# Kernel tuning notes

Measured on AMD Instinct MI355X. Metric: run time of the kernel, lower is better.

## Reference

```python
import jax, jax.numpy as jnp
import numpy as np
from jax import lax

DN = ('NCHW', 'OIHW', 'NCHW')


def setup_inputs() -> dict:
    key = jax.random.key(0)
    k1, k2, k3, k4, k5, k6 = jax.random.split(key, 6)
    B, Ch, H, W = 16, 256, 32, 32   # two feature maps of 256 ch -> c = 512
    C = 2 * Ch
    return {
        'x1': jax.random.normal(k1, (B, Ch, H, W), dtype=jnp.float32),
        'x2': jax.random.normal(k2, (B, Ch, H, W), dtype=jnp.float32),
        'g_w': jax.random.normal(k3, (C, C, 3, 3), dtype=jnp.float32) * 0.02,
        'w_w': jax.random.normal(k4, (256, C, 1, 1), dtype=jnp.float32) * 0.05,
        'weight1': jax.random.normal(k5, (C, 16), dtype=jnp.float32) * 0.1,
        'weight2': jax.random.normal(k6, (C, 16), dtype=jnp.float32) * 0.1,
    }


def reference(x1, x2, g_w, w_w, weight1, weight2):
    x = jnp.concatenate([x1, x2], axis=1)            # [b, c, h, w]
    b, c, h, w = x.shape
    g_x = lax.conv_general_dilated(x, g_w, (1, 1), 'SAME', dimension_numbers=DN)
    value = g_x.reshape(b, c, h * w)                 # [b, c, n]
    q = x.reshape(b, c, h * w)                       # query == key source
    sim = jnp.einsum('bcn,bdn->bcd', q, q) * (float(c) ** -0.5)  # [b, c, c]
    random_map = weight1 @ weight2.T                 # [c, c]
    attn = jax.nn.softmax(sim + random_map[None], axis=-1)
    ctx = jnp.einsum('bcd,bdn->bcn', attn, value).reshape(b, c, h, w)
    out = lax.conv_general_dilated(ctx, w_w, (1, 1), 'VALID', dimension_numbers=DN)
    return out
```

## Files before the change

kernel.cpp:

```cpp
#include <hip/hip_runtime.h>
#include <math.h>

typedef float f32x4 __attribute__((ext_vector_type(4)));
typedef short s16x8 __attribute__((ext_vector_type(8)));
typedef unsigned int u32;
typedef unsigned short u16;
typedef u16 u16x4 __attribute__((ext_vector_type(4)));

static constexpr size_t OFF_XT    = 0;
static constexpr size_t OFF_XQ    = 4734976;
static constexpr size_t OFF_ATTNT = 8929280;
static constexpr size_t OFF_SIMT  = 11026432;
static constexpr size_t OFF_WA    = 13123584;
static constexpr size_t OFF_RM    = 14303232;
static constexpr size_t OFF_WWB   = 14565376;

__device__ __forceinline__ u16 f2bf(float f) {
    u32 u = __float_as_uint(f);
    u32 r = (u + 0x7FFFu + ((u >> 16) & 1u)) >> 16;
    return (u16)r;
}
__device__ __forceinline__ float bf2f(u16 v) {
    return __uint_as_float(((u32)v) << 16);
}

__device__ __forceinline__ void gload_lds16(const void* g, void* l) {
    __builtin_amdgcn_global_load_lds(
        (const u32 __attribute__((address_space(1)))*)(uintptr_t)g,
        (u32 __attribute__((address_space(3)))*)(uintptr_t)l, 16, 0, 0);
}

__global__ __launch_bounds__(256) void prep_kernel(const float* __restrict__ x1,
                                                   const float* __restrict__ x2,
                                                   const float* __restrict__ gw,
                                                   const float* __restrict__ ww,
                                                   const float* __restrict__ w1,
                                                   const float* __restrict__ w2,
                                                   float* __restrict__ rm,
                                                   u16* __restrict__ wA,
                                                   u16* __restrict__ wwb,
                                                   u16* __restrict__ xT,
                                                   u16* __restrict__ xq) {
    __shared__ __attribute__((aligned(16))) u32 shm[4608];
    const int t = threadIdx.x;
    const int bid = blockIdx.x;

    if (bid < 512) {
        const int co = bid;
        const float* g = gw + (size_t)co * 4608;
        float* lf = (float*)shm;
#pragma unroll
        for (int i = 0; i < 18; ++i) lf[t + i * 256] = g[t + i * 256];
        __syncthreads();
        u16* dst = wA + (size_t)co * 4608;
#pragma unroll
        for (int i = 0; i < 18; ++i) {
            int k = t + i * 256;
            int r = k >> 9, ci = k & 511;
            dst[k] = f2bf(lf[ci * 9 + r]);
        }
    } else if (bid < 2560) {
        int xid = bid - 512;
        int nt = xid & 15;
        int cit = (xid >> 4) & 7;
        int b = xid >> 7;
        int n0 = nt * 64, ci0 = cit * 64;
        const float* src = (ci0 < 256) ? (x1 + ((size_t)(b * 256 + ci0)) * 1024)
                                       : (x2 + ((size_t)(b * 256 + ci0 - 256)) * 1024);
        u16* xqb = xq + ((size_t)(b * 512 + ci0)) * 1024;
        u16* lt = (u16*)shm;
#pragma unroll
        for (int p4 = 0; p4 < 4; ++p4) {
            int ch = (t >> 4) + p4 * 16;
            int px = (t & 15) * 4;
            float4 v = *(const float4*)&src[(size_t)ch * 1024 + n0 + px];
            u16x4 pk = {f2bf(v.x), f2bf(v.y), f2bf(v.z), f2bf(v.w)};
            *(u16x4*)&xqb[(size_t)ch * 1024 + n0 + px] = pk;
            lt[(px + 0) * 65 + ch] = pk[0];
            lt[(px + 1) * 65 + ch] = pk[1];
            lt[(px + 2) * 65 + ch] = pk[2];
            lt[(px + 3) * 65 + ch] = pk[3];
        }
        __syncthreads();
        {
            int px_l = t >> 2, c16 = (t & 3) * 16;
            int n = n0 + px_l;
            int y = n >> 5, x = n & 31;
            int p = (y + 1) * 34 + (x + 1);
            u16* dst = xT + ((size_t)b * 1156 + p) * 512 + ci0 + c16;
            *(s16x8*)&dst[0] = *(const s16x8*)&lt[px_l * 65 + c16];
            *(s16x8*)&dst[8] = *(const s16x8*)&lt[px_l * 65 + c16 + 8];
        }
    } else if (bid < 2576) {
        int b = bid - 2560;
        u16* base = xT + (size_t)b * 1156 * 512;
        s16x8 z = {0, 0, 0, 0, 0, 0, 0, 0};
        for (int idx = t; idx < 132 * 64; idx += 256) {
            int row = idx >> 6, seg = idx & 63;
            int p;
            if (row < 34) p = row;
            else if (row < 68) p = 1122 + (row - 34);
            else if (row < 100) p = (row - 67) * 34;
            else p = (row - 99) * 34 + 33;
            *(s16x8*)&base[(size_t)p * 512 + seg * 8] = z;
        }
    } else if (bid < 3600) {
        int idx = (bid - 2576) * 256 + t;
        int c = idx >> 9, d = idx & 511;
        float s = 0.f;
#pragma unroll
        for (int k = 0; k < 16; ++k) s = fmaf(w1[c * 16 + k], w2[d * 16 + k], s);
        rm[idx] = s;
    } else {
        int idx = (bid - 3600) * 256 + t;
        float4 v = ((const float4*)ww)[idx];
        u16x4 pk = {f2bf(v.x), f2bf(v.y), f2bf(v.z), f2bf(v.w)};
        *(u16x4*)&wwb[(size_t)idx * 4] = pk;
    }
}

__global__ __launch_bounds__(256) void sim_gemm(const u16* __restrict__ xq,
                                                const float* __restrict__ rm,
                                                u16* __restrict__ simT) {
    __shared__ __attribute__((aligned(16))) u16 smem[128 * 128];
    u16* As = smem;
    u16* Bs = smem + 128 * 64;
    const int b = blockIdx.z, m0 = blockIdx.y * 128, n0 = blockIdx.x * 128;
    const int t = threadIdx.x, w = t >> 6, l = t & 63;
    const u16* xb = xq + (size_t)b * 512 * 1024;

    const u16 *agp[4], *bgp[4];
    u16 *ald[4], *bld[4];
#pragma unroll
    for (int i = 0; i < 4; ++i) {
        int rr = w * 8 + i * 32 + (l >> 3);
        int gi = (l & 7) ^ (rr & 7);
        agp[i] = xb + (size_t)(m0 + rr) * 1024 + gi * 8;
        bgp[i] = xb + (size_t)(n0 + rr) * 1024 + gi * 8;
        ald[i] = &As[(w * 8 + i * 32) * 64];
        bld[i] = &Bs[(w * 8 + i * 32) * 64];
    }

    f32x4 acc[4][4] = {};
    const int wm = (w >> 1) * 64, wn = (w & 1) * 64;

    for (int kt = 0; kt < 16; ++kt) {
        int ko = kt << 6;
        if (kt) __syncthreads();
#pragma unroll
        for (int i = 0; i < 4; ++i) gload_lds16(agp[i] + ko, ald[i]);
#pragma unroll
        for (int i = 0; i < 4; ++i) gload_lds16(bgp[i] + ko, bld[i]);
        __syncthreads();
#pragma unroll
        for (int kk = 0; kk < 2; ++kk) {
            int gbase = kk * 4 + (l >> 4);
            s16x8 af[4], bf[4];
#pragma unroll
            for (int i = 0; i < 4; ++i) {
                int row = wm + i * 16 + (l & 15);
                af[i] = *(const s16x8*)&As[row * 64 + ((gbase ^ (row & 7)) << 3)];
            }
#pragma unroll
            for (int j = 0; j < 4; ++j) {
                int row = wn + j * 16 + (l & 15);
                bf[j] = *(const s16x8*)&Bs[row * 64 + ((gbase ^ (row & 7)) << 3)];
            }
#pragma unroll
            for (int i = 0; i < 4; ++i)
#pragma unroll
                for (int j = 0; j < 4; ++j)
                    acc[i][j] = __builtin_amdgcn_mfma_f32_16x16x32_bf16(af[i], bf[j], acc[i][j], 0, 0, 0);
        }
    }

    __syncthreads();
    const int col = l & 15, r4 = (l >> 4) * 4;
    const float scale = 0.04419417382415922f;
#pragma unroll
    for (int i = 0; i < 4; ++i)
#pragma unroll
        for (int j = 0; j < 4; ++j) {
            int n_l = wn + j * 16 + col;
            int m_b = wm + i * 16 + r4;
            u16x4 pk;
#pragma unroll
            for (int reg = 0; reg < 4; ++reg) {
                float v = acc[i][j][reg] * scale
                        + rm[(size_t)(m0 + m_b + reg) * 512 + (n0 + n_l)];
                pk[reg] = f2bf(v);
            }
            *(u16x4*)&smem[n_l * 128 + (m_b ^ ((n_l & 15) << 3))] = pk;
        }
    __syncthreads();
    u16* sTb = simT + (size_t)b * 512 * 512;
    {
        int n_l = t >> 1;
#pragma unroll
        for (int rep = 0; rep < 8; ++rep) {
            int c0 = (((t & 1) + rep * 2) << 3);
            s16x8 v = *(const s16x8*)&smem[n_l * 128 + (c0 ^ ((n_l & 15) << 3))];
            *(s16x8*)&sTb[(size_t)(n0 + n_l) * 512 + m0 + c0] = v;
        }
    }
}

__global__ __launch_bounds__(256) void softmax_t(const u16* __restrict__ simT,
                                                 u16* __restrict__ attnT) {
    __shared__ float scr[256];
    const int t = threadIdx.x;
    const int b = blockIdx.x >> 4, c0 = (blockIdx.x & 15) * 32;
    const int cl = t & 31, g = t >> 5;
    const u16* sp = simT + (size_t)b * 512 * 512 + c0 + cl;
    u16* ap = attnT + (size_t)b * 512 * 512 + c0 + cl;

    float s = 0.f;
#pragma unroll 8
    for (int dd = 0; dd < 64; ++dd) {
        int d = g * 64 + dd;
        s += __expf(bf2f(sp[(size_t)d * 512]));
    }
    scr[t] = s;
    __syncthreads();
    float tot = 0.f;
#pragma unroll
    for (int k = 0; k < 8; ++k) tot += scr[k * 32 + cl];
    float inv = 1.f / tot;
#pragma unroll 8
    for (int dd = 0; dd < 64; ++dd) {
        int d = g * 64 + dd;
        float e = __expf(bf2f(sp[(size_t)d * 512])) * inv;
        ap[(size_t)d * 512] = f2bf(e);
    }
}

__global__ __launch_bounds__(256) void conv_gemm(const u16* __restrict__ wA,
                                                 const u16* __restrict__ xT,
                                                 u16* __restrict__ vT) {
    __shared__ __attribute__((aligned(16))) u16 smem[128 * 128];
    u16* As = smem;
    u16* Bs = smem + 128 * 64;
    const int b = blockIdx.z, m0 = blockIdx.y * 128, n0 = blockIdx.x * 128;
    const int t = threadIdx.x, w = t >> 6, l = t & 63;
    const u16* xTb = xT + (size_t)b * 1156 * 512;

    int gi[4], pb[4];
    const u16* agp[4];
    u16 *ald[4], *bld[4];
#pragma unroll
    for (int i = 0; i < 4; ++i) {
        int rr = w * 8 + i * 32 + (l >> 3);
        gi[i] = (l & 7) ^ (rr & 7);
        agp[i] = wA + (size_t)(m0 + rr) * 4608 + gi[i] * 8;
        int n = n0 + rr;
        pb[i] = (n >> 5) * 34 + (n & 31);
        ald[i] = &As[(w * 8 + i * 32) * 64];
        bld[i] = &Bs[(w * 8 + i * 32) * 64];
    }

    f32x4 acc[4][4] = {};
    const int wm = (w >> 1) * 64, wn = (w & 1) * 64;

    for (int kt = 0; kt < 72; ++kt) {
        int r = kt >> 3, ci0k = (kt & 7) << 6;
        int rdiv3 = (r * 11) >> 5;
        int poff = rdiv3 * 34 + (r - rdiv3 * 3);
        int aofs = r * 512 + ci0k;
        if (kt) __syncthreads();
#pragma unroll
        for (int i = 0; i < 4; ++i) gload_lds16(agp[i] + aofs, ald[i]);
#pragma unroll
        for (int i = 0; i < 4; ++i)
            gload_lds16(xTb + (size_t)(pb[i] + poff) * 512 + ci0k + gi[i] * 8, bld[i]);
        __syncthreads();

#pragma unroll
        for (int kk = 0; kk < 2; ++kk) {
            int gbase = kk * 4 + (l >> 4);
            s16x8 af[4], bf[4];
#pragma unroll
            for (int i = 0; i < 4; ++i) {
                int row = wm + i * 16 + (l & 15);
                af[i] = *(const s16x8*)&As[row * 64 + ((gbase ^ (row & 7)) << 3)];
            }
#pragma unroll
            for (int j = 0; j < 4; ++j) {
                int row = wn + j * 16 + (l & 15);
                bf[j] = *(const s16x8*)&Bs[row * 64 + ((gbase ^ (row & 7)) << 3)];
            }
#pragma unroll
            for (int i = 0; i < 4; ++i)
#pragma unroll
                for (int j = 0; j < 4; ++j)
                    acc[i][j] = __builtin_amdgcn_mfma_f32_16x16x32_bf16(af[i], bf[j], acc[i][j], 0, 0, 0);
        }
    }

    __syncthreads();
    const int col = l & 15, r4 = (l >> 4) * 4;
#pragma unroll
    for (int i = 0; i < 4; ++i)
#pragma unroll
        for (int j = 0; j < 4; ++j) {
            int n_l = wn + j * 16 + col;
            int co_b = wm + i * 16 + r4;
            u16x4 pk = {f2bf(acc[i][j][0]), f2bf(acc[i][j][1]),
                        f2bf(acc[i][j][2]), f2bf(acc[i][j][3])};
            *(u16x4*)&smem[n_l * 128 + (co_b ^ ((n_l & 15) << 3))] = pk;
        }
    __syncthreads();
    u16* vTb = vT + (size_t)b * 1024 * 512;
    {
        int n_l = t >> 1;
#pragma unroll
        for (int rep = 0; rep < 8; ++rep) {
            int c0 = (((t & 1) + rep * 2) << 3);
            s16x8 v = *(const s16x8*)&smem[n_l * 128 + (c0 ^ ((n_l & 15) << 3))];
            *(s16x8*)&vTb[(size_t)(n0 + n_l) * 512 + m0 + c0] = v;
        }
    }
}

template <int MODE>
__global__ __launch_bounds__(256) void gemm_nt(const u16* __restrict__ A, size_t sA,
                                               const u16* __restrict__ B, size_t sB,
                                               void* __restrict__ Cv, size_t sC,
                                               int K, int ldc) {
    __shared__ __attribute__((aligned(16))) u16 As[128 * 64];
    __shared__ __attribute__((aligned(16))) u16 Bs[128 * 64];
    const int b = blockIdx.z, m0 = blockIdx.y * 128, n0 = blockIdx.x * 128;
    const int t = threadIdx.x, w = t >> 6, l = t & 63;
    const u16* Ab = A + (size_t)b * sA;
    const u16* Bb = B + (size_t)b * sB;

    const u16 *agp[4], *bgp[4];
    u16 *ald[4], *bld[4];
#pragma unroll
    for (int i = 0; i < 4; ++i) {
        int rr = w * 8 + i * 32 + (l >> 3);
        int gi = (l & 7) ^ (rr & 7);
        agp[i] = Ab + (size_t)(m0 + rr) * K + gi * 8;
        bgp[i] = Bb + (size_t)(n0 + rr) * K + gi * 8;
        ald[i] = &As[(w * 8 + i * 32) * 64];
        bld[i] = &Bs[(w * 8 + i * 32) * 64];
    }

    f32x4 acc[4][4] = {};
    const int wm = (w >> 1) * 64, wn = (w & 1) * 64;
    const int nkt = K >> 6;
    for (int kt = 0; kt < nkt; ++kt) {
        int ko = kt << 6;
        if (kt) __syncthreads();
#pragma unroll
        for (int i = 0; i < 4; ++i) gload_lds16(agp[i] + ko, ald[i]);
#pragma unroll
        for (int i = 0; i < 4; ++i) gload_lds16(bgp[i] + ko, bld[i]);
        __syncthreads();
#pragma unroll
        for (int kk = 0; kk < 2; ++kk) {
            int gbase = kk * 4 + (l >> 4);
            s16x8 af[4], bf[4];
#pragma unroll
            for (int i = 0; i < 4; ++i) {
                int row = wm + i * 16 + (l & 15);
                af[i] = *(const s16x8*)&As[row * 64 + ((gbase ^ (row & 7)) << 3)];
            }
#pragma unroll
            for (int j = 0; j < 4; ++j) {
                int row = wn + j * 16 + (l & 15);
                bf[j] = *(const s16x8*)&Bs[row * 64 + ((gbase ^ (row & 7)) << 3)];
            }
#pragma unroll
            for (int i = 0; i < 4; ++i)
#pragma unroll
                for (int j = 0; j < 4; ++j)
                    acc[i][j] = __builtin_amdgcn_mfma_f32_16x16x32_bf16(af[i], bf[j], acc[i][j], 0, 0, 0);
        }
    }

    const int col = l & 15, r4 = (l >> 4) * 4;
#pragma unroll
    for (int i = 0; i < 4; ++i)
#pragma unroll
        for (int j = 0; j < 4; ++j)
#pragma unroll
            for (int reg = 0; reg < 4; ++reg) {
                int m = m0 + wm + i * 16 + r4 + reg;
                int n = n0 + wn + j * 16 + col;
                if (MODE == 1) {
                    u16* C = (u16*)Cv + (size_t)b * sC;
                    C[(size_t)m * ldc + n] = f2bf(acc[i][j][reg]);
                } else {
                    float* C = (float*)Cv + (size_t)b * sC;
                    C[(size_t)m * ldc + n] = acc[i][j][reg];
                }
            }
}

extern "C" void kernel_launch(void* const* d_in, const int* in_sizes, int n_in,
                              void* d_out, int out_size, void* d_ws, size_t ws_size,
                              hipStream_t stream) {
    (void)in_sizes; (void)n_in; (void)out_size; (void)ws_size;
    const float* x1 = (const float*)d_in[0];
    const float* x2 = (const float*)d_in[1];
    const float* gw = (const float*)d_in[2];
    const float* ww = (const float*)d_in[3];
    const float* w1 = (const float*)d_in[4];
    const float* w2 = (const float*)d_in[5];
    float* out = (float*)d_out;
    float* ws = (float*)d_ws;

    u16* xT    = (u16*)(ws + OFF_XT);
    u16* xq    = (u16*)(ws + OFF_XQ);
    u16* vT    = (u16*)(ws + OFF_XQ);
    u16* attnT = (u16*)(ws + OFF_ATTNT);
    u16* simT  = (u16*)(ws + OFF_SIMT);
    u16* wattn = (u16*)(ws + OFF_SIMT);
    u16* wA    = (u16*)(ws + OFF_WA);
    float* rm  = ws + OFF_RM;
    u16* wwb   = (u16*)(ws + OFF_WWB);

    prep_kernel<<<3728, 256, 0, stream>>>(x1, x2, gw, ww, w1, w2, rm, wA, wwb, xT, xq);
    sim_gemm<<<dim3(4, 4, 16), 256, 0, stream>>>(xq, rm, simT);
    softmax_t<<<256, 256, 0, stream>>>(simT, attnT);
    gemm_nt<1><<<dim3(4, 2, 16), 256, 0, stream>>>(
        wwb, 0, attnT, (size_t)512 * 512, wattn, (size_t)256 * 512, 512, 512);
    conv_gemm<<<dim3(8, 4, 16), 256, 0, stream>>>(wA, xT, vT);
    gemm_nt<2><<<dim3(8, 2, 16), 256, 0, stream>>>(
        wattn, (size_t)256 * 512, vT, (size_t)1024 * 512, out, (size_t)256 * 1024, 512, 1024);
}
```

Before: 234.0 us.

## Split sim GEMM over K into two partials and fuse reduction into softmax

The sim GEMM is split-K into two halves, doubling the grid from 256 to 512 blocks so more CUs are occupied. The partials are written in bf16 and summed in a new finish kernel, which also applies the scale and the random-map bias (staged in LDS) and writes the unnormalized exps once, then rescales them in place. This trades extra partial-sum traffic, an extra bf16 rounding of each partial, and a 64KB LDS tile per block for better GEMM occupancy and one fewer exp pass.

```diff
diff --git a/kernel.cpp b/kernel.cpp
--- a/kernel.cpp
+++ b/kernel.cpp
@@ -9,8 +9,11 @@
 
 static constexpr size_t OFF_XT    = 0;
 static constexpr size_t OFF_XQ    = 4734976;
-static constexpr size_t OFF_ATTNT = 8929280;
-static constexpr size_t OFF_SIMT  = 11026432;
+static constexpr size_t OFF_ATTNT = 4734976;
+static constexpr size_t OFF_WATTN = 6832128;
+static constexpr size_t OFF_P0    = 8929280;
+static constexpr size_t OFF_P1    = 11026432;
+static constexpr size_t OFF_VT    = 8929280;
 static constexpr size_t OFF_WA    = 13123584;
 static constexpr size_t OFF_RM    = 14303232;
 static constexpr size_t OFF_WWB   = 14565376;
@@ -119,15 +122,15 @@
     }
 }
 
-__global__ __launch_bounds__(256) void sim_gemm(const u16* __restrict__ xq,
-                                                const float* __restrict__ rm,
-                                                u16* __restrict__ simT) {
+__global__ __launch_bounds__(256) void sim_part(const u16* __restrict__ xq,
+                                                u16* __restrict__ simP) {
     __shared__ __attribute__((aligned(16))) u16 smem[128 * 128];
     u16* As = smem;
     u16* Bs = smem + 128 * 64;
-    const int b = blockIdx.z, m0 = blockIdx.y * 128, n0 = blockIdx.x * 128;
+    const int b = blockIdx.z, m0 = blockIdx.y * 128;
+    const int n0 = (blockIdx.x & 3) * 128, khalf = blockIdx.x >> 2;
     const int t = threadIdx.x, w = t >> 6, l = t & 63;
-    const u16* xb = xq + (size_t)b * 512 * 1024;
+    const u16* xb = xq + (size_t)b * 512 * 1024 + khalf * 512;
 
     const u16 *agp[4], *bgp[4];
     u16 *ald[4], *bld[4];
@@ -144,7 +147,7 @@
     f32x4 acc[4][4] = {};
     const int wm = (w >> 1) * 64, wn = (w & 1) * 64;
 
-    for (int kt = 0; kt < 16; ++kt) {
+    for (int kt = 0; kt < 8; ++kt) {
         int ko = kt << 6;
         if (kt) __syncthreads();
 #pragma unroll
@@ -176,24 +179,18 @@
 
     __syncthreads();
     const int col = l & 15, r4 = (l >> 4) * 4;
-    const float scale = 0.04419417382415922f;
 #pragma unroll
     for (int i = 0; i < 4; ++i)
 #pragma unroll
         for (int j = 0; j < 4; ++j) {
             int n_l = wn + j * 16 + col;
             int m_b = wm + i * 16 + r4;
-            u16x4 pk;
-#pragma unroll
-            for (int reg = 0; reg < 4; ++reg) {
-                float v = acc[i][j][reg] * scale
-                        + rm[(size_t)(m0 + m_b + reg) * 512 + (n0 + n_l)];
-                pk[reg] = f2bf(v);
-            }
+            u16x4 pk = {f2bf(acc[i][j][0]), f2bf(acc[i][j][1]),
+                        f2bf(acc[i][j][2]), f2bf(acc[i][j][3])};
             *(u16x4*)&smem[n_l * 128 + (m_b ^ ((n_l & 15) << 3))] = pk;
         }
     __syncthreads();
-    u16* sTb = simT + (size_t)b * 512 * 512;
+    u16* sTb = simP + (size_t)khalf * 4194304 + (size_t)b * 512 * 512;
     {
         int n_l = t >> 1;
 #pragma unroll
@@ -205,20 +202,36 @@
     }
 }
 
-__global__ __launch_bounds__(256) void softmax_t(const u16* __restrict__ simT,
-                                                 u16* __restrict__ attnT) {
+__global__ __launch_bounds__(256) void finish_kernel(const u16* __restrict__ p0,
+                                                     const u16* __restrict__ p1,
+                                                     const float* __restrict__ rm,
+                                                     u16* __restrict__ attnT) {
+    __shared__ float rml[32 * 513];
     __shared__ float scr[256];
     const int t = threadIdx.x;
     const int b = blockIdx.x >> 4, c0 = (blockIdx.x & 15) * 32;
     const int cl = t & 31, g = t >> 5;
-    const u16* sp = simT + (size_t)b * 512 * 512 + c0 + cl;
-    u16* ap = attnT + (size_t)b * 512 * 512 + c0 + cl;
+    const float scale = 0.04419417382415922f;
+
+    for (int idx = t; idx < 32 * 512; idx += 256) {
+        int c_l = idx >> 9, d = idx & 511;
+        rml[c_l * 513 + d] = rm[(size_t)(c0 + c_l) * 512 + d];
+    }
+    __syncthreads();
+
+    const u16* q0 = p0 + (size_t)b * 262144 + c0 + cl;
+    const u16* q1 = p1 + (size_t)b * 262144 + c0 + cl;
+    u16* ap = attnT + (size_t)b * 262144 + c0 + cl;
+    const float* rp = &rml[cl * 513];
 
     float s = 0.f;
 #pragma unroll 8
     for (int dd = 0; dd < 64; ++dd) {
         int d = g * 64 + dd;
-        s += __expf(bf2f(sp[(size_t)d * 512]));
+        float v = (bf2f(q0[(size_t)d * 512]) + bf2f(q1[(size_t)d * 512])) * scale + rp[d];
+        float e = __expf(v);
+        s += e;
+        ap[(size_t)d * 512] = f2bf(e);
     }
     scr[t] = s;
     __syncthreads();
@@ -229,8 +242,7 @@
 #pragma unroll 8
     for (int dd = 0; dd < 64; ++dd) {
         int d = g * 64 + dd;
-        float e = __expf(bf2f(sp[(size_t)d * 512])) * inv;
-        ap[(size_t)d * 512] = f2bf(e);
+        ap[(size_t)d * 512] = f2bf(bf2f(ap[(size_t)d * 512]) * inv);
     }
 }
 
@@ -412,17 +424,19 @@
 
     u16* xT    = (u16*)(ws + OFF_XT);
     u16* xq    = (u16*)(ws + OFF_XQ);
-    u16* vT    = (u16*)(ws + OFF_XQ);
     u16* attnT = (u16*)(ws + OFF_ATTNT);
-    u16* simT  = (u16*)(ws + OFF_SIMT);
-    u16* wattn = (u16*)(ws + OFF_SIMT);
+    u16* wattn = (u16*)(ws + OFF_WATTN);
+    u16* simP  = (u16*)(ws + OFF_P0);
+    u16* p0    = (u16*)(ws + OFF_P0);
+    u16* p1    = (u16*)(ws + OFF_P1);
+    u16* vT    = (u16*)(ws + OFF_VT);
     u16* wA    = (u16*)(ws + OFF_WA);
     float* rm  = ws + OFF_RM;
     u16* wwb   = (u16*)(ws + OFF_WWB);
 
     prep_kernel<<<3728, 256, 0, stream>>>(x1, x2, gw, ww, w1, w2, rm, wA, wwb, xT, xq);
-    sim_gemm<<<dim3(4, 4, 16), 256, 0, stream>>>(xq, rm, simT);
-    softmax_t<<<256, 256, 0, stream>>>(simT, attnT);
+    sim_part<<<dim3(8, 4, 16), 256, 0, stream>>>(xq, simP);
+    finish_kernel<<<256, 256, 0, stream>>>(p0, p1, rm, attnT);
     gemm_nt<1><<<dim3(4, 2, 16), 256, 0, stream>>>(
         wwb, 0, attnT, (size_t)512 * 512, wattn, (size_t)256 * 512, 512, 512);
     conv_gemm<<<dim3(8, 4, 16), 256, 0, stream>>>(wA, xT, vT);
```

Measured after the change: 229.9 us. About the same (-1.8%).
